# Optimization experiments

Hardware: AMD Instinct MI355X
Metric: run time of the kernel (lower is better)

## Reference

```python
import jax, jax.numpy as jnp
import numpy as np

B, C, H, W = 2, 256, 32, 32
NUM_HEADS = 8
HEAD_DIM = C // NUM_HEADS
SCALE = HEAD_DIM ** -0.5
K1, K2 = 2, 3
KERNELS = [3, 5, 7]
STRIDES = [1, 1, 1]
PADS = [1, 2, 3]


def avgpool2d(y, k, s, p):
    # PyTorch AvgPool2d default count_include_pad=True: divide by k*k always
    yp = jnp.pad(y, ((0, 0), (0, 0), (p, p), (p, p)))
    summed = jax.lax.reduce_window(yp, 0.0, jax.lax.add,
                                   (1, 1, k, k), (1, 1, s, s), 'VALID')
    return summed / float(k * k)


def layer_norm(x, g, b, eps=1e-5):
    mu = jnp.mean(x, axis=-1, keepdims=True)
    var = jnp.var(x, axis=-1, keepdims=True)
    return (x - mu) / jnp.sqrt(var + eps) * g + b


def topk_mask(attn, kk):
    # boolean mask with True at the top-kk positions along the last axis
    idx = jax.lax.top_k(attn, kk)[1]                     # [B,h,N,kk]
    mask = jnp.zeros(attn.shape, dtype=bool)
    return jnp.put_along_axis(mask, idx, True, axis=-1, inplace=False)


def setup_inputs() -> dict:
    key = jax.random.key(0)
    ks = jax.random.split(key, 8)
    std = 1.0 / np.sqrt(C)
    return {
        'x': jax.random.normal(ks[0], (B, C, H, W), jnp.float32),
        'y': jax.random.normal(ks[1], (B, C, H, W), jnp.float32),
        'Wq': jax.random.uniform(ks[2], (C, C), jnp.float32, -std, std),
        'Wkv': jax.random.uniform(ks[3], (2 * C, C), jnp.float32, -std, std),
        'Wproj': jax.random.uniform(ks[4], (C, C), jnp.float32, -std, std),
        'bproj': jax.random.uniform(ks[5], (C,), jnp.float32, -std, std),
        'ln_g': jnp.ones((C,), jnp.float32),
        'ln_b': jnp.zeros((C,), jnp.float32),
        'attn1_p': jnp.full((1,), 0.5, jnp.float32),
        'attn2_p': jnp.full((1,), 0.5, jnp.float32),
    }


def reference(x, y, Wq, Wkv, Wproj, bproj, ln_g, ln_b, attn1_p, attn2_p):
    # multi-scale average pooling fusion of y (stride 1 keeps H,W)
    yf = (avgpool2d(y, KERNELS[0], STRIDES[0], PADS[0])
          + avgpool2d(y, KERNELS[1], STRIDES[1], PADS[1])
          + avgpool2d(y, KERNELS[2], STRIDES[2], PADS[2]))
    yf = yf.reshape(B, C, H * W).transpose(0, 2, 1)      # [B, N1, C]
    yf = layer_norm(yf, ln_g, ln_b)
    N1 = yf.shape[1]

    kv = yf @ Wkv.T                                      # [B, N1, 2C]
    kv = kv.reshape(B, N1, 2, NUM_HEADS, HEAD_DIM).transpose(2, 0, 3, 1, 4)
    k, v = kv[0], kv[1]                                  # [B, h, N1, d]

    xf = x.reshape(B, C, H * W).transpose(0, 2, 1)       # [B, N, C]
    N = xf.shape[1]
    q = (xf @ Wq.T).reshape(B, N, NUM_HEADS, HEAD_DIM).transpose(0, 2, 1, 3)

    attn = jnp.einsum('bhnd,bhmd->bhnm', q, k) * SCALE   # [B, h, N, N1]

    neg_inf = jnp.array(-jnp.inf, attn.dtype)
    m1 = topk_mask(attn, int(N1 / K1))
    a1 = jax.nn.softmax(jnp.where(m1, attn, neg_inf), axis=-1)
    out1 = jnp.einsum('bhnm,bhmd->bhnd', a1, v)

    m2 = topk_mask(attn, int(N1 / K2))
    a2 = jax.nn.softmax(jnp.where(m2, attn, neg_inf), axis=-1)
    out2 = jnp.einsum('bhnm,bhmd->bhnd', a2, v)

    out = out1 * attn1_p + out2 * attn2_p                # [B, h, N, d]
    out = out.transpose(0, 2, 1, 3).reshape(B, N, C)
    out = out @ Wproj.T + bproj
    hw = int(np.sqrt(N))
    return out.transpose(0, 2, 1).reshape(B, C, hw, hw)
```

## Files before the change

### kernel.cpp

```cpp
#include <hip/hip_runtime.h>

typedef _Float16 f16;
typedef f16 f16x8 __attribute__((ext_vector_type(8)));
typedef f16 f16x4 __attribute__((ext_vector_type(4)));
typedef float f32x4 __attribute__((ext_vector_type(4)));

constexpr float ATT_SCALE = 0.17677669529663687f;

template<int C> __device__ __forceinline__ float dppadd(float v) {
    return v + __int_as_float(__builtin_amdgcn_update_dpp(0, __float_as_int(v), C, 0xf, 0xf, true));
}
template<int C> __device__ __forceinline__ float dppmax(float v) {
    return fmaxf(v, __int_as_float(__builtin_amdgcn_update_dpp(__float_as_int(v), __float_as_int(v), C, 0xf, 0xf, false)));
}
template<int C> __device__ __forceinline__ float dppmin(float v) {
    return fminf(v, __int_as_float(__builtin_amdgcn_update_dpp(__float_as_int(v), __float_as_int(v), C, 0xf, 0xf, false)));
}
__device__ __forceinline__ float wave_sum(float v) {
    v = dppadd<0x111>(v); v = dppadd<0x112>(v); v = dppadd<0x114>(v); v = dppadd<0x118>(v);
    v = dppadd<0x142>(v); v = dppadd<0x143>(v);
    return __int_as_float(__builtin_amdgcn_readlane(__float_as_int(v), 63));
}
__device__ __forceinline__ float wave_max(float v) {
    v = dppmax<0x111>(v); v = dppmax<0x112>(v); v = dppmax<0x114>(v); v = dppmax<0x118>(v);
    v = dppmax<0x142>(v); v = dppmax<0x143>(v);
    return __int_as_float(__builtin_amdgcn_readlane(__float_as_int(v), 63));
}
__device__ __forceinline__ float wave_min(float v) {
    v = dppmin<0x111>(v); v = dppmin<0x112>(v); v = dppmin<0x114>(v); v = dppmin<0x118>(v);
    v = dppmin<0x142>(v); v = dppmin<0x143>(v);
    return __int_as_float(__builtin_amdgcn_readlane(__float_as_int(v), 63));
}

__global__ __launch_bounds__(256) void prep_kernel(const float* __restrict__ y,
                                                   float* __restrict__ pooled,
                                                   const float* __restrict__ x,
                                                   f16* __restrict__ xT,
                                                   const float* __restrict__ Wq,
                                                   const float* __restrict__ Wkv,
                                                   const float* __restrict__ Wp,
                                                   f16* __restrict__ wq16,
                                                   f16* __restrict__ wkv16,
                                                   f16* __restrict__ wp16)
{
    __shared__ float sh[1444];
    int bid = blockIdx.x, t = threadIdx.x;
    if (bid < 512) {
        float (*p)[38] = (float(*)[38])sh;
        const float* plane = y + (size_t)bid * 1024;
        for (int i = t; i < 38 * 38; i += 256) (&p[0][0])[i] = 0.f;
        __syncthreads();
        for (int i = t; i < 1024; i += 256) p[(i >> 5) + 3][(i & 31) + 3] = plane[i];
        __syncthreads();
        int b = bid >> 8, c = bid & 255;
        for (int i = t; i < 1024; i += 256) {
            int r = (i >> 5) + 3, cc = (i & 31) + 3;
            float s3 = 0.f;
            #pragma unroll
            for (int dr = -1; dr <= 1; ++dr)
                #pragma unroll
                for (int dc = -1; dc <= 1; ++dc) s3 += p[r + dr][cc + dc];
            float r5 = 0.f;
            #pragma unroll
            for (int dc = -2; dc <= 2; ++dc) r5 += p[r - 2][cc + dc] + p[r + 2][cc + dc];
            #pragma unroll
            for (int dr = -1; dr <= 1; ++dr) r5 += p[r + dr][cc - 2] + p[r + dr][cc + 2];
            float r7 = 0.f;
            #pragma unroll
            for (int dc = -3; dc <= 3; ++dc) r7 += p[r - 3][cc + dc] + p[r + 3][cc + dc];
            #pragma unroll
            for (int dr = -2; dr <= 2; ++dr) r7 += p[r + dr][cc - 3] + p[r + dr][cc + 3];
            float s5 = s3 + r5, s7 = s5 + r7;
            pooled[((size_t)b * 1024 + i) * 256 + c] =
                s3 * (1.f / 9.f) + s5 * (1.f / 25.f) + s7 * (1.f / 49.f);
        }
    } else if (bid < 1024) {
        float (*tile)[33] = (float(*)[33])sh;
        int id = bid - 512;
        int b = id >> 8, ct = (id >> 5) & 7, nt = id & 31;
        int rr = t >> 5, j = t & 31;
        #pragma unroll
        for (int r = rr; r < 32; r += 8)
            tile[r][j] = x[((size_t)b * 256 + ct * 32 + r) * 1024 + nt * 32 + j];
        __syncthreads();
        #pragma unroll
        for (int r = rr; r < 32; r += 8)
            xT[((size_t)b * 1024 + nt * 32 + r) * 256 + ct * 32 + j] = (f16)tile[j][r];
    } else {
        int i = (bid - 1024) * 256 + t;
        if (i < 65536) { wq16[i] = (f16)Wq[i]; wp16[i] = (f16)Wp[i]; }
        wkv16[i] = (f16)Wkv[i];
    }
}

__global__ __launch_bounds__(256) void ln_kernel(const float* __restrict__ pooled,
                                                 const float* __restrict__ g,
                                                 const float* __restrict__ bta,
                                                 f16* __restrict__ yfln)
{
    int w = threadIdx.x >> 6, lane = threadIdx.x & 63;
    int row = blockIdx.x * 4 + w;
    float4 v = ((const float4*)(pooled + (size_t)row * 256))[lane];
    float s  = v.x + v.y + v.z + v.w;
    float s2 = v.x * v.x + v.y * v.y + v.z * v.z + v.w * v.w;
    s = wave_sum(s); s2 = wave_sum(s2);
    float mu = s * (1.f / 256.f);
    float var = s2 * (1.f / 256.f) - mu * mu;
    float rstd = rsqrtf(var + 1e-5f);
    float4 gg = ((const float4*)g)[lane];
    float4 bb = ((const float4*)bta)[lane];
    f16x4 o;
    o[0] = (f16)((v.x - mu) * rstd * gg.x + bb.x);
    o[1] = (f16)((v.y - mu) * rstd * gg.y + bb.y);
    o[2] = (f16)((v.z - mu) * rstd * gg.z + bb.z);
    o[3] = (f16)((v.w - mu) * rstd * gg.w + bb.w);
    *(f16x4*)(yfln + (size_t)row * 256 + lane * 4) = o;
}

__device__ __forceinline__ void gemm_tile(const f16* __restrict__ A, const f16* __restrict__ Bm,
                                          int row0, int ncol0, int l15, int lhi, f32x4 acc[4])
{
    for (int k0 = 0; k0 < 256; k0 += 32) {
        f16x8 a = *(const f16x8*)(A + (size_t)(row0 + l15) * 256 + k0 + lhi * 8);
        #pragma unroll
        for (int j = 0; j < 4; ++j) {
            f16x8 bf = *(const f16x8*)(Bm + (size_t)(ncol0 + j * 16 + l15) * 256 + k0 + lhi * 8);
            acc[j] = __builtin_amdgcn_mfma_f32_16x16x32_f16(a, bf, acc[j], 0, 0, 0);
        }
    }
}

__global__ __launch_bounds__(256) void qkv_kernel(const f16* __restrict__ xT,
                                                  const f16* __restrict__ yfln,
                                                  const f16* __restrict__ wq16,
                                                  const f16* __restrict__ wkv16,
                                                  f16* __restrict__ q16,
                                                  f16* __restrict__ k16,
                                                  f16* __restrict__ vT16)
{
    int w = threadIdx.x >> 6, lane = threadIdx.x & 63;
    int l15 = lane & 15, lhi = lane >> 4;
    if (blockIdx.x < 128) {
        int mt = blockIdx.x >> 2, nt = blockIdx.x & 3;
        int row0 = mt * 64 + w * 16;
        f32x4 acc[4] = {};
        gemm_tile(xT, wq16, row0, nt * 64, l15, lhi, acc);
        #pragma unroll
        for (int j = 0; j < 4; ++j) {
            int col = nt * 64 + j * 16 + l15;
            int h = col >> 5, d = col & 31;
            #pragma unroll
            for (int r = 0; r < 4; ++r) {
                int row = row0 + 4 * lhi + r;
                int b = row >> 10, n = row & 1023;
                q16[(((size_t)(b * 8 + h)) * 1024 + n) * 32 + d] = (f16)(acc[j][r] * ATT_SCALE);
            }
        }
    } else {
        int bid = blockIdx.x - 128;
        int mt = bid >> 3, nt = bid & 7;
        int row0 = mt * 64 + w * 16;
        f32x4 acc[4] = {};
        gemm_tile(yfln, wkv16, row0, nt * 64, l15, lhi, acc);
        #pragma unroll
        for (int j = 0; j < 4; ++j) {
            int col = nt * 64 + j * 16 + l15;
            #pragma unroll
            for (int r = 0; r < 4; ++r) {
                int row = row0 + 4 * lhi + r;
                int b = row >> 10, n = row & 1023;
                float v = acc[j][r];
                if (col < 256) {
                    int h = col >> 5, d = col & 31;
                    k16[(((size_t)(b * 8 + h)) * 1024 + n) * 32 + d] = (f16)v;
                } else {
                    int c2 = col - 256, h = c2 >> 5, d = c2 & 31;
                    vT16[(((size_t)(b * 8 + h)) * 32 + d) * 1024 + n] = (f16)v;
                }
            }
        }
    }
}

__global__ __launch_bounds__(1024, 8) void attn_kernel(const f16* __restrict__ q16,
                                                       const f16* __restrict__ k16,
                                                       const f16* __restrict__ vT16,
                                                       const float* __restrict__ a1p,
                                                       const float* __restrict__ a2p,
                                                       f16* __restrict__ oat)
{
    __shared__ float Sb[16 * 1024];
    int bid = blockIdx.x;
    int bh = bid >> 6, rb = bid & 63;
    int row0 = rb * 16;
    int w = threadIdx.x >> 6, lane = threadIdx.x & 63;
    int l15 = lane & 15, lhi = lane >> 4;
    const f16* Qb = q16 + (size_t)bh * 32768;
    const f16* Kb = k16 + (size_t)bh * 32768;
    const f16* Vb = vT16 + (size_t)bh * 32768;

    {
        f16x8 qf = *(const f16x8*)(Qb + (size_t)(row0 + l15) * 32 + lhi * 8);
        int q = l15, sw1 = (q & 7) << 2;
        #pragma unroll
        for (int j = 0; j < 4; ++j) {
            int c0 = w * 64 + j * 16;
            f16x8 kf = *(const f16x8*)(Kb + (size_t)(c0 + l15) * 32 + lhi * 8);
            f32x4 z = {0.f, 0.f, 0.f, 0.f};
            f32x4 d = __builtin_amdgcn_mfma_f32_16x16x32_f16(kf, qf, z, 0, 0, 0);
            int k0 = c0 + 4 * lhi;
            *(float4*)&Sb[q * 1024 + (k0 ^ sw1)] = *(float4*)&d;
        }
    }
    __syncthreads();

    float c_a1 = a1p[0], c_a2 = a2p[0];
    int r = w, sw = (r & 7) << 2;
    float s[16];
    #pragma unroll
    for (int i = 0; i < 4; ++i) {
        float4 v4 = *(const float4*)&Sb[r * 1024 + ((256 * i + 4 * lane) ^ sw)];
        s[4 * i + 0] = v4.x; s[4 * i + 1] = v4.y; s[4 * i + 2] = v4.z; s[4 * i + 3] = v4.w;
    }
    float mxl = s[0], mnl = s[0];
    #pragma unroll
    for (int i = 1; i < 16; ++i) { mxl = fmaxf(mxl, s[i]); mnl = fminf(mnl, s[i]); }
    float mx = wave_max(mxl), mn = wave_min(mnl);

    float lo1 = mn, hi1 = mx, lo2 = mn, hi2 = mx;
    float cl1 = 1024.f, ch1 = 1.f, cl2 = 1024.f, ch2 = 1.f;
    bool f1 = false, f2 = false;
    for (int it = 0; it < 16; ++it) {
        if (f1 && f2) break;
        float m1 = lo1, m2 = lo2;
        bool t1 = !f1, t2 = !f2;
        if (t1) {
            m1 = ((it & 3) == 3) ? 0.5f * (lo1 + hi1)
               : lo1 + (hi1 - lo1) * (cl1 - 512.f) * __builtin_amdgcn_rcpf(cl1 - ch1);
            if (!(m1 > lo1 && m1 < hi1)) m1 = 0.5f * (lo1 + hi1);
            if (!(m1 > lo1 && m1 < hi1)) { f1 = true; t1 = false; m1 = lo1; }
        }
        if (t2) {
            m2 = ((it & 3) == 3) ? 0.5f * (lo2 + hi2)
               : lo2 + (hi2 - lo2) * (cl2 - 341.f) * __builtin_amdgcn_rcpf(cl2 - ch2);
            if (!(m2 > lo2 && m2 < hi2)) m2 = 0.5f * (lo2 + hi2);
            if (!(m2 > lo2 && m2 < hi2)) { f2 = true; t2 = false; m2 = lo2; }
        }
        if (!t1 && !t2) break;
        int c1 = 0, c2 = 0;
        #pragma unroll
        for (int i = 0; i < 16; ++i) {
            c1 += (int)__popcll(__ballot(s[i] >= m1));
            c2 += (int)__popcll(__ballot(s[i] >= m2));
        }
        if (t1) {
            if (c1 == 512) { f1 = true; lo1 = m1; }
            else if (c1 > 512) { lo1 = m1; cl1 = (float)c1; }
            else { hi1 = m1; ch1 = (float)c1; }
        }
        if (t2) {
            if (c2 == 341) { f2 = true; lo2 = m2; }
            else if (c2 > 341) { lo2 = m2; cl2 = (float)c2; }
            else { hi2 = m2; ch2 = (float)c2; }
        }
    }
    float T1 = lo1, T2 = lo2;

    float e[16];
    float l1 = 0.f, l2 = 0.f;
    #pragma unroll
    for (int i = 0; i < 16; ++i) {
        float ev = __expf(s[i] - mx);
        e[i] = ev;
        l1 += (s[i] >= T1) ? ev : 0.f;
        l2 += (s[i] >= T2) ? ev : 0.f;
    }
    l1 = wave_sum(l1); l2 = wave_sum(l2);
    float c1w = c_a1 / l1, c2w = c_a2 / l2;
    #pragma unroll
    for (int i = 0; i < 4; ++i) {
        float4 o4;
        float wt;
        wt = (s[4*i+0] >= T1 ? c1w : 0.f) + (s[4*i+0] >= T2 ? c2w : 0.f); o4.x = e[4*i+0] * wt;
        wt = (s[4*i+1] >= T1 ? c1w : 0.f) + (s[4*i+1] >= T2 ? c2w : 0.f); o4.y = e[4*i+1] * wt;
        wt = (s[4*i+2] >= T1 ? c1w : 0.f) + (s[4*i+2] >= T2 ? c2w : 0.f); o4.z = e[4*i+2] * wt;
        wt = (s[4*i+3] >= T1 ? c1w : 0.f) + (s[4*i+3] >= T2 ? c2w : 0.f); o4.w = e[4*i+3] * wt;
        *(float4*)&Sb[r * 1024 + ((256 * i + 4 * lane) ^ sw)] = o4;
    }
    __syncthreads();

    f32x4 acc0 = {}, acc1 = {};
    int swl = (l15 & 7) << 2;
    #pragma unroll
    for (int ks = 0; ks < 2; ++ks) {
        int m0 = w * 64 + ks * 32 + lhi * 8;
        float4 ch0 = *(const float4*)&Sb[l15 * 1024 + ((m0)     ^ swl)];
        float4 ch1 = *(const float4*)&Sb[l15 * 1024 + ((m0 + 4) ^ swl)];
        f16x8 af;
        af[0] = (f16)ch0.x; af[1] = (f16)ch0.y; af[2] = (f16)ch0.z; af[3] = (f16)ch0.w;
        af[4] = (f16)ch1.x; af[5] = (f16)ch1.y; af[6] = (f16)ch1.z; af[7] = (f16)ch1.w;
        f16x8 b0 = *(const f16x8*)(Vb + (size_t)(l15) * 1024 + m0);
        f16x8 b1v = *(const f16x8*)(Vb + (size_t)(16 + l15) * 1024 + m0);
        acc0 = __builtin_amdgcn_mfma_f32_16x16x32_f16(af, b0, acc0, 0, 0, 0);
        acc1 = __builtin_amdgcn_mfma_f32_16x16x32_f16(af, b1v, acc1, 0, 0, 0);
    }
    __syncthreads();
    #pragma unroll
    for (int rr2 = 0; rr2 < 4; ++rr2) {
        int rw = 4 * lhi + rr2;
        Sb[w * 512 + rw * 32 + l15]      = acc0[rr2];
        Sb[w * 512 + rw * 32 + 16 + l15] = acc1[rr2];
    }
    __syncthreads();
    if (threadIdx.x < 128) {
        int o4 = threadIdx.x << 2;
        float4 v = *(const float4*)&Sb[o4];
        #pragma unroll
        for (int ww = 1; ww < 16; ++ww) {
            float4 p = *(const float4*)&Sb[ww * 512 + o4];
            v.x += p.x; v.y += p.y; v.z += p.z; v.w += p.w;
        }
        int rr = o4 >> 5, d0 = o4 & 31;
        int b = bh >> 3, h = bh & 7;
        f16x4 o;
        o[0] = (f16)v.x; o[1] = (f16)v.y; o[2] = (f16)v.z; o[3] = (f16)v.w;
        *(f16x4*)(oat + ((size_t)b * 1024 + row0 + rr) * 256 + h * 32 + d0) = o;
    }
}

__global__ __launch_bounds__(256) void projgemm_kernel(const f16* __restrict__ A,
                                                       const f16* __restrict__ Bm,
                                                       const float* __restrict__ bias,
                                                       float* __restrict__ out)
{
    __shared__ float tile[64][65];
    int mt = blockIdx.x >> 2, nt = blockIdx.x & 3;
    int w = threadIdx.x >> 6, lane = threadIdx.x & 63;
    int l15 = lane & 15, lhi = lane >> 4;
    int row0 = mt * 64 + w * 16;
    f32x4 acc[4] = {};
    gemm_tile(A, Bm, row0, nt * 64, l15, lhi, acc);
    #pragma unroll
    for (int j = 0; j < 4; ++j) {
        int col_l = j * 16 + l15;
        float bv = bias[nt * 64 + col_l];
        #pragma unroll
        for (int r = 0; r < 4; ++r)
            tile[col_l][w * 16 + 4 * lhi + r] = acc[j][r] + bv;
    }
    __syncthreads();
    int b = (mt * 64) >> 10, n0 = (mt * 64) & 1023;
    int col_l = threadIdx.x >> 2, part = threadIdx.x & 3;
    size_t base = (size_t)b * 262144 + (size_t)(nt * 64 + col_l) * 1024 + n0 + part * 16;
    #pragma unroll
    for (int q = 0; q < 4; ++q) {
        float4 v;
        v.x = tile[col_l][part * 16 + q * 4 + 0];
        v.y = tile[col_l][part * 16 + q * 4 + 1];
        v.z = tile[col_l][part * 16 + q * 4 + 2];
        v.w = tile[col_l][part * 16 + q * 4 + 3];
        *(float4*)(out + base + q * 4) = v;
    }
}

extern "C" void kernel_launch(void* const* d_in, const int* in_sizes, int n_in,
                              void* d_out, int out_size, void* d_ws, size_t ws_size,
                              hipStream_t stream)
{
    const float* x     = (const float*)d_in[0];
    const float* y     = (const float*)d_in[1];
    const float* Wq    = (const float*)d_in[2];
    const float* Wkv   = (const float*)d_in[3];
    const float* Wproj = (const float*)d_in[4];
    const float* bproj = (const float*)d_in[5];
    const float* ln_g  = (const float*)d_in[6];
    const float* ln_b  = (const float*)d_in[7];
    const float* a1p   = (const float*)d_in[8];
    const float* a2p   = (const float*)d_in[9];
    float* out = (float*)d_out;

    char* wsb = (char*)d_ws;
    float* pooled = (float*)(wsb);
    f16* yfln  = (f16*)(wsb + ((size_t)2 << 20));
    f16* xT    = (f16*)(wsb + ((size_t)3 << 20));
    f16* wq16  = (f16*)(wsb + ((size_t)4 << 20));
    f16* wkv16 = (f16*)(wsb + ((size_t)4 << 20) + (128 << 10));
    f16* wp16  = (f16*)(wsb + ((size_t)4 << 20) + (384 << 10));
    f16* q16   = (f16*)(wsb + ((size_t)4 << 20) + (512 << 10));
    f16* k16   = (f16*)(wsb + ((size_t)4 << 20) + (512 << 10) + ((size_t)1 << 20));
    f16* vT16  = (f16*)(wsb + ((size_t)4 << 20) + (512 << 10) + ((size_t)2 << 20));
    f16* oat   = (f16*)(wsb + ((size_t)4 << 20) + (512 << 10) + ((size_t)3 << 20));

    prep_kernel<<<1536, 256, 0, stream>>>(y, pooled, x, xT, Wq, Wkv, Wproj,
                                          wq16, wkv16, wp16);
    ln_kernel<<<512, 256, 0, stream>>>(pooled, ln_g, ln_b, yfln);
    qkv_kernel<<<384, 256, 0, stream>>>(xT, yfln, wq16, wkv16, q16, k16, vT16);
    attn_kernel<<<1024, 1024, 0, stream>>>(q16, k16, vT16, a1p, a2p, oat);
    projgemm_kernel<<<128, 256, 0, stream>>>(oat, wp16, bproj, out);
}
```

Measured before the change: 77.90 us.

## Fuse LayerNorm into KV GEMM and seed top-k threshold search with Gaussian estimate

Removes the separate LayerNorm kernel launch. Each KV GEMM block now normalizes its 64 rows of pooled data into a swizzled shared-memory tile before running the MFMA loop, which recomputes the LN for each of the 8 column tiles. In attention, the per-row top-k threshold search is seeded from the row mean and standard deviation, with initial brackets placed around Gaussian quantile guesses, so the interpolation/bisection loop should converge in fewer ballot-count passes. It also recomputes exp instead of holding 16 values in registers, trading ALU work for lower register pressure.

```diff
diff --git a/kernel.cpp b/kernel.cpp
--- a/kernel.cpp
+++ b/kernel.cpp
@@ -93,30 +93,6 @@
     }
 }
 
-__global__ __launch_bounds__(256) void ln_kernel(const float* __restrict__ pooled,
-                                                 const float* __restrict__ g,
-                                                 const float* __restrict__ bta,
-                                                 f16* __restrict__ yfln)
-{
-    int w = threadIdx.x >> 6, lane = threadIdx.x & 63;
-    int row = blockIdx.x * 4 + w;
-    float4 v = ((const float4*)(pooled + (size_t)row * 256))[lane];
-    float s  = v.x + v.y + v.z + v.w;
-    float s2 = v.x * v.x + v.y * v.y + v.z * v.z + v.w * v.w;
-    s = wave_sum(s); s2 = wave_sum(s2);
-    float mu = s * (1.f / 256.f);
-    float var = s2 * (1.f / 256.f) - mu * mu;
-    float rstd = rsqrtf(var + 1e-5f);
-    float4 gg = ((const float4*)g)[lane];
-    float4 bb = ((const float4*)bta)[lane];
-    f16x4 o;
-    o[0] = (f16)((v.x - mu) * rstd * gg.x + bb.x);
-    o[1] = (f16)((v.y - mu) * rstd * gg.y + bb.y);
-    o[2] = (f16)((v.z - mu) * rstd * gg.z + bb.z);
-    o[3] = (f16)((v.w - mu) * rstd * gg.w + bb.w);
-    *(f16x4*)(yfln + (size_t)row * 256 + lane * 4) = o;
-}
-
 __device__ __forceinline__ void gemm_tile(const f16* __restrict__ A, const f16* __restrict__ Bm,
                                           int row0, int ncol0, int l15, int lhi, f32x4 acc[4])
 {
@@ -131,13 +107,16 @@
 }
 
 __global__ __launch_bounds__(256) void qkv_kernel(const f16* __restrict__ xT,
-                                                  const f16* __restrict__ yfln,
+                                                  const float* __restrict__ pooled,
+                                                  const float* __restrict__ lng,
+                                                  const float* __restrict__ lnb,
                                                   const f16* __restrict__ wq16,
                                                   const f16* __restrict__ wkv16,
                                                   f16* __restrict__ q16,
                                                   f16* __restrict__ k16,
                                                   f16* __restrict__ vT16)
 {
+    __shared__ f16 At[64 * 256];
     int w = threadIdx.x >> 6, lane = threadIdx.x & 63;
     int l15 = lane & 15, lhi = lane >> 4;
     if (blockIdx.x < 128) {
@@ -159,15 +138,42 @@
     } else {
         int bid = blockIdx.x - 128;
         int mt = bid >> 3, nt = bid & 7;
-        int row0 = mt * 64 + w * 16;
+        int row0g = mt * 64;
+        float4 gg = ((const float4*)lng)[lane];
+        float4 bb = ((const float4*)lnb)[lane];
+        for (int rr = 0; rr < 16; ++rr) {
+            int r = w * 16 + rr;
+            float4 v = *(const float4*)(pooled + (size_t)(row0g + r) * 256 + lane * 4);
+            float su = v.x + v.y + v.z + v.w;
+            float s2 = v.x * v.x + v.y * v.y + v.z * v.z + v.w * v.w;
+            su = wave_sum(su); s2 = wave_sum(s2);
+            float muv = su * (1.f / 256.f);
+            float rstd = rsqrtf(s2 * (1.f / 256.f) - muv * muv + 1e-5f);
+            f16x4 o;
+            o[0] = (f16)((v.x - muv) * rstd * gg.x + bb.x);
+            o[1] = (f16)((v.y - muv) * rstd * gg.y + bb.y);
+            o[2] = (f16)((v.z - muv) * rstd * gg.z + bb.z);
+            o[3] = (f16)((v.w - muv) * rstd * gg.w + bb.w);
+            *(f16x4*)(At + r * 256 + ((lane * 4) ^ ((r & 7) << 3))) = o;
+        }
+        __syncthreads();
         f32x4 acc[4] = {};
-        gemm_tile(yfln, wkv16, row0, nt * 64, l15, lhi, acc);
+        int a_r = w * 16 + l15;
+        int asw = (a_r & 7) << 3;
+        for (int k0 = 0; k0 < 256; k0 += 32) {
+            f16x8 a = *(const f16x8*)(At + a_r * 256 + ((k0 + lhi * 8) ^ asw));
+            #pragma unroll
+            for (int j = 0; j < 4; ++j) {
+                f16x8 bf = *(const f16x8*)(wkv16 + (size_t)(nt * 64 + j * 16 + l15) * 256 + k0 + lhi * 8);
+                acc[j] = __builtin_amdgcn_mfma_f32_16x16x32_f16(a, bf, acc[j], 0, 0, 0);
+            }
+        }
         #pragma unroll
         for (int j = 0; j < 4; ++j) {
             int col = nt * 64 + j * 16 + l15;
             #pragma unroll
             for (int r = 0; r < 4; ++r) {
-                int row = row0 + 4 * lhi + r;
+                int row = row0g + w * 16 + 4 * lhi + r;
                 int b = row >> 10, n = row & 1023;
                 float v = acc[j][r];
                 if (col < 256) {
@@ -222,36 +228,67 @@
         float4 v4 = *(const float4*)&Sb[r * 1024 + ((256 * i + 4 * lane) ^ sw)];
         s[4 * i + 0] = v4.x; s[4 * i + 1] = v4.y; s[4 * i + 2] = v4.z; s[4 * i + 3] = v4.w;
     }
-    float mxl = s[0], mnl = s[0];
-    #pragma unroll
-    for (int i = 1; i < 16; ++i) { mxl = fmaxf(mxl, s[i]); mnl = fminf(mnl, s[i]); }
+    float mxl = s[0], mnl = s[0], sul = 0.f, s2l = 0.f;
+    #pragma unroll
+    for (int i = 0; i < 16; ++i) {
+        mxl = fmaxf(mxl, s[i]); mnl = fminf(mnl, s[i]);
+        sul += s[i]; s2l += s[i] * s[i];
+    }
     float mx = wave_max(mxl), mn = wave_min(mnl);
-
-    float lo1 = mn, hi1 = mx, lo2 = mn, hi2 = mx;
-    float cl1 = 1024.f, ch1 = 1.f, cl2 = 1024.f, ch2 = 1.f;
+    float mu = wave_sum(sul) * (1.f / 1024.f);
+    float s2m = wave_sum(s2l) * (1.f / 1024.f);
+    float sg = sqrtf(fmaxf(s2m - mu * mu, 1e-30f));
+
+    float a1 = mu - 0.20f * sg, b1 = mu + 0.20f * sg;
+    float g2 = mu + 0.4316f * sg;
+    float a2 = g2 - 0.20f * sg, b2 = g2 + 0.20f * sg;
+    int ca1 = 0, cb1 = 0, ca2 = 0, cb2 = 0;
+    #pragma unroll
+    for (int i = 0; i < 16; ++i) {
+        ca1 += (int)__popcll(__ballot(s[i] >= a1));
+        cb1 += (int)__popcll(__ballot(s[i] >= b1));
+        ca2 += (int)__popcll(__ballot(s[i] >= a2));
+        cb2 += (int)__popcll(__ballot(s[i] >= b2));
+    }
     bool f1 = false, f2 = false;
-    for (int it = 0; it < 16; ++it) {
+    float lo1, hi1 = mx, cl1 = 1024.f, ch1 = 1.f;
+    float lo2, hi2 = mx, cl2 = 1024.f, ch2 = 1.f;
+    if (ca1 == 512)      { f1 = true; lo1 = a1; }
+    else if (cb1 == 512) { f1 = true; lo1 = b1; }
+    else if (ca1 < 512)  { lo1 = mn; cl1 = 1024.f; hi1 = a1; ch1 = (float)ca1; }
+    else if (cb1 >= 512) { lo1 = b1; cl1 = (float)cb1; hi1 = mx; ch1 = 1.f; }
+    else                 { lo1 = a1; cl1 = (float)ca1; hi1 = b1; ch1 = (float)cb1; }
+    if (ca2 == 341)      { f2 = true; lo2 = a2; }
+    else if (cb2 == 341) { f2 = true; lo2 = b2; }
+    else if (ca2 < 341)  { lo2 = mn; cl2 = 1024.f; hi2 = a2; ch2 = (float)ca2; }
+    else if (cb2 >= 341) { lo2 = b2; cl2 = (float)cb2; hi2 = mx; ch2 = 1.f; }
+    else                 { lo2 = a2; cl2 = (float)ca2; hi2 = b2; ch2 = (float)cb2; }
+
+    for (int it = 0; it < 20; ++it) {
         if (f1 && f2) break;
+        bool t1 = !f1, t2 = !f2;
         float m1 = lo1, m2 = lo2;
-        bool t1 = !f1, t2 = !f2;
         if (t1) {
-            m1 = ((it & 3) == 3) ? 0.5f * (lo1 + hi1)
-               : lo1 + (hi1 - lo1) * (cl1 - 512.f) * __builtin_amdgcn_rcpf(cl1 - ch1);
+            m1 = ((it % 3) == 2) ? (0.5f * (lo1 + hi1))
+                                 : (lo1 + (hi1 - lo1) * (cl1 - 512.f) / (cl1 - ch1));
             if (!(m1 > lo1 && m1 < hi1)) m1 = 0.5f * (lo1 + hi1);
-            if (!(m1 > lo1 && m1 < hi1)) { f1 = true; t1 = false; m1 = lo1; }
+            if (!(m1 > lo1 && m1 < hi1)) { f1 = true; t1 = false; }
         }
         if (t2) {
-            m2 = ((it & 3) == 3) ? 0.5f * (lo2 + hi2)
-               : lo2 + (hi2 - lo2) * (cl2 - 341.f) * __builtin_amdgcn_rcpf(cl2 - ch2);
+            m2 = ((it % 3) == 2) ? (0.5f * (lo2 + hi2))
+                                 : (lo2 + (hi2 - lo2) * (cl2 - 341.f) / (cl2 - ch2));
             if (!(m2 > lo2 && m2 < hi2)) m2 = 0.5f * (lo2 + hi2);
-            if (!(m2 > lo2 && m2 < hi2)) { f2 = true; t2 = false; m2 = lo2; }
-        }
-        if (!t1 && !t2) break;
+            if (!(m2 > lo2 && m2 < hi2)) { f2 = true; t2 = false; }
+        }
+        if (!t1 && !t2) continue;
         int c1 = 0, c2 = 0;
-        #pragma unroll
-        for (int i = 0; i < 16; ++i) {
-            c1 += (int)__popcll(__ballot(s[i] >= m1));
-            c2 += (int)__popcll(__ballot(s[i] >= m2));
+        if (t1) {
+            #pragma unroll
+            for (int i = 0; i < 16; ++i) c1 += (int)__popcll(__ballot(s[i] >= m1));
+        }
+        if (t2) {
+            #pragma unroll
+            for (int i = 0; i < 16; ++i) c2 += (int)__popcll(__ballot(s[i] >= m2));
         }
         if (t1) {
             if (c1 == 512) { f1 = true; lo1 = m1; }
@@ -266,12 +303,10 @@
     }
     float T1 = lo1, T2 = lo2;
 
-    float e[16];
     float l1 = 0.f, l2 = 0.f;
     #pragma unroll
     for (int i = 0; i < 16; ++i) {
         float ev = __expf(s[i] - mx);
-        e[i] = ev;
         l1 += (s[i] >= T1) ? ev : 0.f;
         l2 += (s[i] >= T2) ? ev : 0.f;
     }
@@ -280,11 +315,15 @@
     #pragma unroll
     for (int i = 0; i < 4; ++i) {
         float4 o4;
-        float wt;
-        wt = (s[4*i+0] >= T1 ? c1w : 0.f) + (s[4*i+0] >= T2 ? c2w : 0.f); o4.x = e[4*i+0] * wt;
-        wt = (s[4*i+1] >= T1 ? c1w : 0.f) + (s[4*i+1] >= T2 ? c2w : 0.f); o4.y = e[4*i+1] * wt;
-        wt = (s[4*i+2] >= T1 ? c1w : 0.f) + (s[4*i+2] >= T2 ? c2w : 0.f); o4.z = e[4*i+2] * wt;
-        wt = (s[4*i+3] >= T1 ? c1w : 0.f) + (s[4*i+3] >= T2 ? c2w : 0.f); o4.w = e[4*i+3] * wt;
+        float ev, wt;
+        ev = __expf(s[4*i+0] - mx);
+        wt = (s[4*i+0] >= T1 ? c1w : 0.f) + (s[4*i+0] >= T2 ? c2w : 0.f); o4.x = ev * wt;
+        ev = __expf(s[4*i+1] - mx);
+        wt = (s[4*i+1] >= T1 ? c1w : 0.f) + (s[4*i+1] >= T2 ? c2w : 0.f); o4.y = ev * wt;
+        ev = __expf(s[4*i+2] - mx);
+        wt = (s[4*i+2] >= T1 ? c1w : 0.f) + (s[4*i+2] >= T2 ? c2w : 0.f); o4.z = ev * wt;
+        ev = __expf(s[4*i+3] - mx);
+        wt = (s[4*i+3] >= T1 ? c1w : 0.f) + (s[4*i+3] >= T2 ? c2w : 0.f); o4.w = ev * wt;
         *(float4*)&Sb[r * 1024 + ((256 * i + 4 * lane) ^ sw)] = o4;
     }
     __syncthreads();
@@ -381,20 +420,19 @@
 
     char* wsb = (char*)d_ws;
     float* pooled = (float*)(wsb);
-    f16* yfln  = (f16*)(wsb + ((size_t)2 << 20));
-    f16* xT    = (f16*)(wsb + ((size_t)3 << 20));
-    f16* wq16  = (f16*)(wsb + ((size_t)4 << 20));
-    f16* wkv16 = (f16*)(wsb + ((size_t)4 << 20) + (128 << 10));
-    f16* wp16  = (f16*)(wsb + ((size_t)4 << 20) + (384 << 10));
-    f16* q16   = (f16*)(wsb + ((size_t)4 << 20) + (512 << 10));
-    f16* k16   = (f16*)(wsb + ((size_t)4 << 20) + (512 << 10) + ((size_t)1 << 20));
-    f16* vT16  = (f16*)(wsb + ((size_t)4 << 20) + (512 << 10) + ((size_t)2 << 20));
-    f16* oat   = (f16*)(wsb + ((size_t)4 << 20) + (512 << 10) + ((size_t)3 << 20));
+    f16* xT    = (f16*)(wsb + ((size_t)2 << 20));
+    f16* wq16  = (f16*)(wsb + ((size_t)3 << 20));
+    f16* wkv16 = (f16*)(wsb + ((size_t)3 << 20) + (128 << 10));
+    f16* wp16  = (f16*)(wsb + ((size_t)3 << 20) + (384 << 10));
+    f16* q16   = (f16*)(wsb + ((size_t)3 << 20) + (512 << 10));
+    f16* k16   = (f16*)(wsb + ((size_t)3 << 20) + (512 << 10) + ((size_t)1 << 20));
+    f16* vT16  = (f16*)(wsb + ((size_t)3 << 20) + (512 << 10) + ((size_t)2 << 20));
+    f16* oat   = (f16*)(wsb + ((size_t)3 << 20) + (512 << 10) + ((size_t)3 << 20));
 
     prep_kernel<<<1536, 256, 0, stream>>>(y, pooled, x, xT, Wq, Wkv, Wproj,
                                           wq16, wkv16, wp16);
-    ln_kernel<<<512, 256, 0, stream>>>(pooled, ln_g, ln_b, yfln);
-    qkv_kernel<<<384, 256, 0, stream>>>(xT, yfln, wq16, wkv16, q16, k16, vT16);
+    qkv_kernel<<<384, 256, 0, stream>>>(xT, pooled, ln_g, ln_b, wq16, wkv16,
+                                        q16, k16, vT16);
     attn_kernel<<<1024, 1024, 0, stream>>>(q16, k16, vT16, a1p, a2p, oat);
     projgemm_kernel<<<128, 256, 0, stream>>>(oat, wp16, bproj, out);
 }
```

Result: slower. 79.51 us (+2.1%).
